# Kernel tuning notes

Hardware: AMD Instinct MI355X
Metric: run time of the kernel (lower is better)

The kernel has to match this reference:

```python
import jax, jax.numpy as jnp
import numpy as np

N_NODES = 100000
N_EDGES = 1600000
IN_FEATS = 64
HIDDEN = 64
NUM_CLASSES = 16


def setup_inputs() -> dict:
    key = jax.random.key(0)
    ks = jax.random.split(key, 8)
    features = jax.random.normal(ks[0], (N_NODES, IN_FEATS), dtype=jnp.float32)
    src = jax.random.randint(ks[1], (N_EDGES,), 0, N_NODES, dtype=jnp.int64)
    dst = jax.random.randint(ks[2], (N_EDGES,), 0, N_NODES, dtype=jnp.int64)
    W1 = jax.random.normal(ks[3], (IN_FEATS, HIDDEN), dtype=jnp.float32) * (1.0 / np.sqrt(IN_FEATS))
    b1 = jax.random.normal(ks[4], (HIDDEN,), dtype=jnp.float32) * 0.01
    W2 = jax.random.normal(ks[5], (HIDDEN, NUM_CLASSES), dtype=jnp.float32) * (1.0 / np.sqrt(HIDDEN))
    b2 = jax.random.normal(ks[6], (NUM_CLASSES,), dtype=jnp.float32) * 0.01
    return {"features": features, "src": src, "dst": dst,
            "W1": W1, "b1": b1, "W2": W2, "b2": b2}


def _mean_aggregate(x, src, dst, n_nodes):
    # gather source features along edges, segment-sum into destinations
    msg_sum = jax.ops.segment_sum(x[src], dst, num_segments=n_nodes)  # [N, d]
    deg = jax.ops.segment_sum(jnp.ones_like(dst, dtype=x.dtype), dst,
                              num_segments=n_nodes)                   # [N]
    # DGL mean leaves zero-in-degree nodes at 0; sum is already 0 there,
    # so clamping degree to 1 is exact.
    return msg_sum / jnp.maximum(deg, 1.0)[:, None]


def reference(features, src, dst, W1, b1, W2, b2):
    n = features.shape[0]
    h = _mean_aggregate(features, src, dst, n) @ W1 + b1   # GCNLayer 1
    h = jax.nn.relu(h)
    out = _mean_aggregate(h, src, dst, n) @ W2 + b2        # GCNLayer 2
    return out
```

## Files before the change

kernel.cpp:

```cpp
#include <hip/hip_runtime.h>
#include <hip/hip_fp16.h>

static constexpr int F = 64;
static constexpr int C = 16;
static constexpr int EPB = 2048;
static constexpr int BSH = 9;
static constexpr int SRCB = 17;
static constexpr int NPG = 4;

__global__ void prep(const float* __restrict__ x, __half* __restrict__ xh, int n4,
                     const int* __restrict__ dst, int* __restrict__ bucketCount,
                     int* __restrict__ blockHist, int nEdges) {
    int stride = gridDim.x * blockDim.x;
    for (int i = blockIdx.x * blockDim.x + threadIdx.x; i < n4; i += stride) {
        float4 v = ((const float4*)x)[i];
        __half2 p0 = __floats2half2_rn(v.x, v.y);
        __half2 p1 = __floats2half2_rn(v.z, v.w);
        uint2 o;
        o.x = *reinterpret_cast<unsigned*>(&p0);
        o.y = *reinterpret_cast<unsigned*>(&p1);
        ((uint2*)xh)[i] = o;
    }
    __shared__ int h[256];
    int t = threadIdx.x;
    h[t] = 0;
    __syncthreads();
    int e0 = blockIdx.x * EPB;
    for (int i = 0; i < EPB / 256; ++i) {
        int e = e0 + i * 256 + t;
        if (e < nEdges) atomicAdd(&h[dst[e] >> BSH], 1);
    }
    __syncthreads();
    blockHist[blockIdx.x * 256 + t] = h[t] ? atomicAdd(&bucketCount[t], h[t]) : 0;
}

__global__ void bucket_scan(const int* __restrict__ bucketCount,
                            int* __restrict__ bucketStart) {
    __shared__ int s[256];
    int t = threadIdx.x;
    s[t] = bucketCount[t];
    __syncthreads();
    for (int o = 1; o < 256; o <<= 1) {
        int v = (t >= o) ? s[t - o] : 0;
        __syncthreads();
        s[t] += v;
        __syncthreads();
    }
    bucketStart[t] = (t > 0) ? s[t - 1] : 0;
    if (t == 255) bucketStart[256] = s[255];
}

__global__ void partition(const int* __restrict__ src, const int* __restrict__ dst,
                          const int* __restrict__ blockHist,
                          const int* __restrict__ bucketStart,
                          unsigned* __restrict__ pairs, int nEdges) {
    __shared__ int base[256];
    __shared__ int rank[256];
    int t = threadIdx.x;
    rank[t] = 0;
    base[t] = bucketStart[t] + blockHist[blockIdx.x * 256 + t];
    __syncthreads();
    int e0 = blockIdx.x * EPB;
    for (int i = 0; i < EPB / 256; ++i) {
        int e = e0 + i * 256 + t;
        if (e < nEdges) {
            int d = dst[e];
            int b = d >> BSH;
            int r = atomicAdd(&rank[b], 1);
            pairs[base[b] + r] =
                ((unsigned)(d & ((1 << BSH) - 1)) << SRCB) | (unsigned)src[e];
        }
    }
}

__global__ void bucket_csr(const unsigned* __restrict__ pairs,
                           const int* __restrict__ bucketStart,
                           int* __restrict__ rowstart, int* __restrict__ csr,
                           int nNodes, int nEdges) {
    __shared__ int cnt[512];
    __shared__ int s[512];
    __shared__ int cur[512];
    int t = threadIdx.x;
    int b = blockIdx.x;
    int nodeBase = b << BSH;
    int pBeg = bucketStart[b], pEnd = bucketStart[b + 1];
    cnt[t] = 0;
    __syncthreads();
    for (int i = pBeg + t; i < pEnd; i += 512)
        atomicAdd(&cnt[pairs[i] >> SRCB], 1);
    __syncthreads();
    s[t] = cnt[t];
    __syncthreads();
    for (int o = 1; o < 512; o <<= 1) {
        int v = (t >= o) ? s[t - o] : 0;
        __syncthreads();
        s[t] += v;
        __syncthreads();
    }
    int rs = pBeg + ((t > 0) ? s[t - 1] : 0);
    int node = nodeBase + t;
    if (node < nNodes) rowstart[node] = rs;
    cur[t] = rs;
    __syncthreads();
    for (int i = pBeg + t; i < pEnd; i += 512) {
        unsigned p = pairs[i];
        int pos = atomicAdd(&cur[p >> SRCB], 1);
        csr[pos] = (int)(p & ((1u << SRCB) - 1));
    }
    if (b == 0 && t == 0) rowstart[nNodes] = nEdges;
}

__global__ void gather_h2(const __half* __restrict__ xh,
                          const int* __restrict__ rowstart,
                          const int* __restrict__ csr,
                          float* __restrict__ agg, int nNodes) {
    int gid = (blockIdx.x * blockDim.x + threadIdx.x) >> 4;
    int q = threadIdx.x & 15;
    int nodeBase = gid * NPG;
    if (nodeBase >= nNodes) return;
    const uint2* x2 = (const uint2*)xh;
    int rs[NPG + 1];
#pragma unroll
    for (int i = 0; i <= NPG; ++i) rs[i] = rowstart[min(nodeBase + i, nNodes)];
#pragma unroll
    for (int i = 0; i < NPG; ++i) {
        int node = nodeBase + i;
        if (node >= nNodes) break;
        int beg = rs[i], end = rs[i + 1];
        float4 a0 = make_float4(0.f, 0.f, 0.f, 0.f);
        float4 a1 = make_float4(0.f, 0.f, 0.f, 0.f);
        float4 a2 = make_float4(0.f, 0.f, 0.f, 0.f);
        float4 a3 = make_float4(0.f, 0.f, 0.f, 0.f);
        int k = beg;
        for (; k + 4 <= end; k += 4) {
            int s0 = csr[k], s1 = csr[k + 1], s2 = csr[k + 2], s3 = csr[k + 3];
            uint2 u0 = x2[(size_t)s0 * 16 + q];
            uint2 u1 = x2[(size_t)s1 * 16 + q];
            uint2 u2 = x2[(size_t)s2 * 16 + q];
            uint2 u3 = x2[(size_t)s3 * 16 + q];
            __half2 h00 = *reinterpret_cast<__half2*>(&u0.x);
            __half2 h01 = *reinterpret_cast<__half2*>(&u0.y);
            a0.x += __low2float(h00); a0.y += __high2float(h00);
            a0.z += __low2float(h01); a0.w += __high2float(h01);
            __half2 h10 = *reinterpret_cast<__half2*>(&u1.x);
            __half2 h11 = *reinterpret_cast<__half2*>(&u1.y);
            a1.x += __low2float(h10); a1.y += __high2float(h10);
            a1.z += __low2float(h11); a1.w += __high2float(h11);
            __half2 h20 = *reinterpret_cast<__half2*>(&u2.x);
            __half2 h21 = *reinterpret_cast<__half2*>(&u2.y);
            a2.x += __low2float(h20); a2.y += __high2float(h20);
            a2.z += __low2float(h21); a2.w += __high2float(h21);
            __half2 h30 = *reinterpret_cast<__half2*>(&u3.x);
            __half2 h31 = *reinterpret_cast<__half2*>(&u3.y);
            a3.x += __low2float(h30); a3.y += __high2float(h30);
            a3.z += __low2float(h31); a3.w += __high2float(h31);
        }
        for (; k < end; ++k) {
            int s0 = csr[k];
            uint2 u0 = x2[(size_t)s0 * 16 + q];
            __half2 h00 = *reinterpret_cast<__half2*>(&u0.x);
            __half2 h01 = *reinterpret_cast<__half2*>(&u0.y);
            a0.x += __low2float(h00); a0.y += __high2float(h00);
            a0.z += __low2float(h01); a0.w += __high2float(h01);
        }
        float inv = 1.0f / fmaxf((float)(end - beg), 1.0f);
        float4 o;
        o.x = ((a0.x + a1.x) + (a2.x + a3.x)) * inv;
        o.y = ((a0.y + a1.y) + (a2.y + a3.y)) * inv;
        o.z = ((a0.z + a1.z) + (a2.z + a3.z)) * inv;
        o.w = ((a0.w + a1.w) + (a2.w + a3.w)) * inv;
        ((float4*)agg)[(size_t)node * 16 + q] = o;
    }
}

__global__ void dense12_reg(const float* __restrict__ agg,
                            const float* __restrict__ W1,
                            const float* __restrict__ b1,
                            const float* __restrict__ W2,
                            __half* __restrict__ t2, int nNodes) {
    __shared__ float xs[4][F];
    __shared__ float hs[4][F];
    __shared__ float red[4][4][17];
    int wave = threadIdx.x >> 6, lane = threadIdx.x & 63;
    int kk = lane >> 4, c = lane & 15;

    float w1[F];
#pragma unroll
    for (int k = 0; k < F; ++k) w1[k] = W1[k * F + lane];
    float b1l = b1[lane];
    float w2[16];
#pragma unroll
    for (int j = 0; j < 16; ++j) w2[j] = W2[(kk * 16 + j) * C + c];

    int step = gridDim.x * 4;
    int start = blockIdx.x * 4 + wave;
    int iters = (nNodes + step - 1) / step;
    for (int i = 0; i < iters; ++i) {
        int node = start + i * step;
        bool live = node < nNodes;
        xs[wave][lane] = live ? agg[(size_t)node * F + lane] : 0.0f;
        __syncthreads();
        float hacc = b1l;
#pragma unroll
        for (int k = 0; k < F; ++k) hacc = fmaf(xs[wave][k], w1[k], hacc);
        hs[wave][lane] = fmaxf(hacc, 0.0f);
        __syncthreads();
        float p = 0.0f;
#pragma unroll
        for (int j = 0; j < 16; ++j) p = fmaf(hs[wave][kk * 16 + j], w2[j], p);
        red[wave][kk][c] = p;
        __syncthreads();
        if (lane < C && live) {
            float o = red[wave][0][lane] + red[wave][1][lane]
                    + red[wave][2][lane] + red[wave][3][lane];
            t2[(size_t)node * C + lane] = __float2half_rn(o);
        }
        __syncthreads();
    }
}

__global__ void gather16c(const __half* __restrict__ t2,
                          const int* __restrict__ rowstart,
                          const int* __restrict__ csr,
                          const float* __restrict__ b2,
                          float* __restrict__ out, int nNodes) {
    int gid = (blockIdx.x * blockDim.x + threadIdx.x) >> 4;
    int c = threadIdx.x & 15;
    int nodeBase = gid * NPG;
    if (nodeBase >= nNodes) return;
    float b2c = b2[c];
    int rs[NPG + 1];
#pragma unroll
    for (int i = 0; i <= NPG; ++i) rs[i] = rowstart[min(nodeBase + i, nNodes)];
#pragma unroll
    for (int i = 0; i < NPG; ++i) {
        int node = nodeBase + i;
        if (node >= nNodes) break;
        int beg = rs[i], end = rs[i + 1];
        float a0 = 0.f, a1 = 0.f, a2 = 0.f, a3 = 0.f;
        int k = beg;
        for (; k + 4 <= end; k += 4) {
            int s0 = csr[k], s1 = csr[k + 1], s2 = csr[k + 2], s3 = csr[k + 3];
            a0 += __half2float(t2[(size_t)s0 * C + c]);
            a1 += __half2float(t2[(size_t)s1 * C + c]);
            a2 += __half2float(t2[(size_t)s2 * C + c]);
            a3 += __half2float(t2[(size_t)s3 * C + c]);
        }
        for (; k < end; ++k) a0 += __half2float(t2[(size_t)csr[k] * C + c]);
        float d = fmaxf((float)(end - beg), 1.0f);
        out[(size_t)node * C + c] = ((a0 + a1) + (a2 + a3)) / d + b2c;
    }
}

extern "C" void kernel_launch(void* const* d_in, const int* in_sizes, int n_in,
                              void* d_out, int out_size, void* d_ws, size_t ws_size,
                              hipStream_t stream) {
    const float* features = (const float*)d_in[0];
    const int*   src      = (const int*)d_in[1];
    const int*   dst      = (const int*)d_in[2];
    const float* W1       = (const float*)d_in[3];
    const float* b1       = (const float*)d_in[4];
    const float* W2       = (const float*)d_in[5];
    const float* b2       = (const float*)d_in[6];
    float*       out      = (float*)d_out;

    const int nNodes = in_sizes[0] / F;
    const int nEdges = in_sizes[1];
    const int NBUCK = (nNodes + 511) >> BSH;
    const int NBLK  = (nEdges + EPB - 1) / EPB;

    char* ws = (char*)d_ws;
    auto align = [](size_t x) { return (x + 255) / 256 * 256; };
    int* bucketCount  = (int*)ws;    ws += align(256 * 4);
    int* bucketStart  = (int*)ws;    ws += align(257 * 4);
    int* blockHist    = (int*)ws;    ws += align((size_t)NBLK * 256 * 4);
    int* rowstart     = (int*)ws;    ws += align((size_t)(nNodes + 1) * 4);
    int* csr          = (int*)ws;    ws += align((size_t)nEdges * 4);
    __half* xh        = (__half*)ws; ws += align((size_t)nNodes * F * 2);
    float* agg        = (float*)ws;  ws += align((size_t)nNodes * F * 4);
    __half* t2h       = (__half*)ws; ws += align((size_t)nNodes * C * 2);
    unsigned* pairs   = (unsigned*)agg;

    hipMemsetAsync(bucketCount, 0, 256 * sizeof(int), stream);

    prep<<<NBLK, 256, 0, stream>>>(features, xh, nNodes * F / 4,
                                   dst, bucketCount, blockHist, nEdges);
    bucket_scan<<<1, 256, 0, stream>>>(bucketCount, bucketStart);
    partition<<<NBLK, 256, 0, stream>>>(src, dst, blockHist, bucketStart, pairs, nEdges);
    bucket_csr<<<NBUCK, 512, 0, stream>>>(pairs, bucketStart, rowstart, csr,
                                          nNodes, nEdges);

    {
        int nGroups = (nNodes + NPG - 1) / NPG;
        int blocks = (nGroups * 16 + 255) / 256;
        gather_h2<<<blocks, 256, 0, stream>>>(xh, rowstart, csr, agg, nNodes);
    }
    dense12_reg<<<2048, 256, 0, stream>>>(agg, W1, b1, W2, t2h, nNodes);

    {
        int nGroups = (nNodes + NPG - 1) / NPG;
        int blocks = (nGroups * 16 + 255) / 256;
        gather16c<<<blocks, 256, 0, stream>>>(t2h, rowstart, csr, b2, out, nNodes);
    }
}
```

Before: 151.7 us.

## Fold bucket scan into consumers and widen per-lane gather loads

Removes the single-block bucket_scan launch by recomputing the 256-entry prefix scan redundantly inside every partition and bucket_csr block. Both gather kernels now use wider per-lane loads: 16-byte half8 for layer 1 with 8 lanes per node, and 8-byte half4 for layer 2 with 4 lanes per node and float4 stores. The aim is fewer launches and fewer, larger memory transactions per gathered row. In exchange each block does extra scan work and barriers, and fewer threads per node means less parallelism per edge list.

```diff
diff --git a/kernel.cpp b/kernel.cpp
--- a/kernel.cpp
+++ b/kernel.cpp
@@ -34,31 +34,25 @@
     blockHist[blockIdx.x * 256 + t] = h[t] ? atomicAdd(&bucketCount[t], h[t]) : 0;
 }
 
-__global__ void bucket_scan(const int* __restrict__ bucketCount,
-                            int* __restrict__ bucketStart) {
-    __shared__ int s[256];
-    int t = threadIdx.x;
-    s[t] = bucketCount[t];
-    __syncthreads();
-    for (int o = 1; o < 256; o <<= 1) {
-        int v = (t >= o) ? s[t - o] : 0;
-        __syncthreads();
-        s[t] += v;
-        __syncthreads();
-    }
-    bucketStart[t] = (t > 0) ? s[t - 1] : 0;
-    if (t == 255) bucketStart[256] = s[255];
-}
-
 __global__ void partition(const int* __restrict__ src, const int* __restrict__ dst,
                           const int* __restrict__ blockHist,
-                          const int* __restrict__ bucketStart,
+                          const int* __restrict__ bucketCount,
                           unsigned* __restrict__ pairs, int nEdges) {
+    __shared__ int s[256];
     __shared__ int base[256];
     __shared__ int rank[256];
     int t = threadIdx.x;
+    s[t] = bucketCount[t];
     rank[t] = 0;
-    base[t] = bucketStart[t] + blockHist[blockIdx.x * 256 + t];
+    __syncthreads();
+    for (int o = 1; o < 256; o <<= 1) {
+        int v = (t >= o) ? s[t - o] : 0;
+        __syncthreads();
+        s[t] += v;
+        __syncthreads();
+    }
+    int bstart = (t > 0) ? s[t - 1] : 0;
+    base[t] = bstart + blockHist[blockIdx.x * 256 + t];
     __syncthreads();
     int e0 = blockIdx.x * EPB;
     for (int i = 0; i < EPB / 256; ++i) {
@@ -74,16 +68,26 @@
 }
 
 __global__ void bucket_csr(const unsigned* __restrict__ pairs,
-                           const int* __restrict__ bucketStart,
+                           const int* __restrict__ bucketCount,
                            int* __restrict__ rowstart, int* __restrict__ csr,
                            int nNodes, int nEdges) {
+    __shared__ int bscan[256];
     __shared__ int cnt[512];
     __shared__ int s[512];
     __shared__ int cur[512];
     int t = threadIdx.x;
     int b = blockIdx.x;
+    if (t < 256) bscan[t] = bucketCount[t];
+    __syncthreads();
+    for (int o = 1; o < 256; o <<= 1) {
+        int v = (t < 256 && t >= o) ? bscan[t - o] : 0;
+        __syncthreads();
+        if (t < 256) bscan[t] += v;
+        __syncthreads();
+    }
+    int pBeg = (b > 0) ? bscan[b - 1] : 0;
+    int pEnd = bscan[b];
     int nodeBase = b << BSH;
-    int pBeg = bucketStart[b], pEnd = bucketStart[b + 1];
     cnt[t] = 0;
     __syncthreads();
     for (int i = pBeg + t; i < pEnd; i += 512)
@@ -110,15 +114,26 @@
     if (b == 0 && t == 0) rowstart[nNodes] = nEdges;
 }
 
-__global__ void gather_h2(const __half* __restrict__ xh,
+__device__ __forceinline__ void acc8(float* a, uint4 u) {
+    __half2 h0 = *reinterpret_cast<__half2*>(&u.x);
+    __half2 h1 = *reinterpret_cast<__half2*>(&u.y);
+    __half2 h2 = *reinterpret_cast<__half2*>(&u.z);
+    __half2 h3 = *reinterpret_cast<__half2*>(&u.w);
+    a[0] += __low2float(h0); a[1] += __high2float(h0);
+    a[2] += __low2float(h1); a[3] += __high2float(h1);
+    a[4] += __low2float(h2); a[5] += __high2float(h2);
+    a[6] += __low2float(h3); a[7] += __high2float(h3);
+}
+
+__global__ void gather_h8(const __half* __restrict__ xh,
                           const int* __restrict__ rowstart,
                           const int* __restrict__ csr,
                           float* __restrict__ agg, int nNodes) {
-    int gid = (blockIdx.x * blockDim.x + threadIdx.x) >> 4;
-    int q = threadIdx.x & 15;
+    int gid = (blockIdx.x * blockDim.x + threadIdx.x) >> 3;
+    int q = threadIdx.x & 7;
     int nodeBase = gid * NPG;
     if (nodeBase >= nNodes) return;
-    const uint2* x2 = (const uint2*)xh;
+    const uint4* x4 = (const uint4*)xh;
     int rs[NPG + 1];
 #pragma unroll
     for (int i = 0; i <= NPG; ++i) rs[i] = rowstart[min(nodeBase + i, nNodes)];
@@ -127,49 +142,33 @@
         int node = nodeBase + i;
         if (node >= nNodes) break;
         int beg = rs[i], end = rs[i + 1];
-        float4 a0 = make_float4(0.f, 0.f, 0.f, 0.f);
-        float4 a1 = make_float4(0.f, 0.f, 0.f, 0.f);
-        float4 a2 = make_float4(0.f, 0.f, 0.f, 0.f);
-        float4 a3 = make_float4(0.f, 0.f, 0.f, 0.f);
+        float a0[8] = {0,0,0,0,0,0,0,0};
+        float a1[8] = {0,0,0,0,0,0,0,0};
+        float a2[8] = {0,0,0,0,0,0,0,0};
+        float a3[8] = {0,0,0,0,0,0,0,0};
         int k = beg;
         for (; k + 4 <= end; k += 4) {
             int s0 = csr[k], s1 = csr[k + 1], s2 = csr[k + 2], s3 = csr[k + 3];
-            uint2 u0 = x2[(size_t)s0 * 16 + q];
-            uint2 u1 = x2[(size_t)s1 * 16 + q];
-            uint2 u2 = x2[(size_t)s2 * 16 + q];
-            uint2 u3 = x2[(size_t)s3 * 16 + q];
-            __half2 h00 = *reinterpret_cast<__half2*>(&u0.x);
-            __half2 h01 = *reinterpret_cast<__half2*>(&u0.y);
-            a0.x += __low2float(h00); a0.y += __high2float(h00);
-            a0.z += __low2float(h01); a0.w += __high2float(h01);
-            __half2 h10 = *reinterpret_cast<__half2*>(&u1.x);
-            __half2 h11 = *reinterpret_cast<__half2*>(&u1.y);
-            a1.x += __low2float(h10); a1.y += __high2float(h10);
-            a1.z += __low2float(h11); a1.w += __high2float(h11);
-            __half2 h20 = *reinterpret_cast<__half2*>(&u2.x);
-            __half2 h21 = *reinterpret_cast<__half2*>(&u2.y);
-            a2.x += __low2float(h20); a2.y += __high2float(h20);
-            a2.z += __low2float(h21); a2.w += __high2float(h21);
-            __half2 h30 = *reinterpret_cast<__half2*>(&u3.x);
-            __half2 h31 = *reinterpret_cast<__half2*>(&u3.y);
-            a3.x += __low2float(h30); a3.y += __high2float(h30);
-            a3.z += __low2float(h31); a3.w += __high2float(h31);
-        }
-        for (; k < end; ++k) {
-            int s0 = csr[k];
-            uint2 u0 = x2[(size_t)s0 * 16 + q];
-            __half2 h00 = *reinterpret_cast<__half2*>(&u0.x);
-            __half2 h01 = *reinterpret_cast<__half2*>(&u0.y);
-            a0.x += __low2float(h00); a0.y += __high2float(h00);
-            a0.z += __low2float(h01); a0.w += __high2float(h01);
-        }
+            uint4 u0 = x4[(size_t)s0 * 8 + q];
+            uint4 u1 = x4[(size_t)s1 * 8 + q];
+            uint4 u2 = x4[(size_t)s2 * 8 + q];
+            uint4 u3 = x4[(size_t)s3 * 8 + q];
+            acc8(a0, u0); acc8(a1, u1); acc8(a2, u2); acc8(a3, u3);
+        }
+        for (; k < end; ++k)
+            acc8(a0, x4[(size_t)csr[k] * 8 + q]);
         float inv = 1.0f / fmaxf((float)(end - beg), 1.0f);
-        float4 o;
-        o.x = ((a0.x + a1.x) + (a2.x + a3.x)) * inv;
-        o.y = ((a0.y + a1.y) + (a2.y + a3.y)) * inv;
-        o.z = ((a0.z + a1.z) + (a2.z + a3.z)) * inv;
-        o.w = ((a0.w + a1.w) + (a2.w + a3.w)) * inv;
-        ((float4*)agg)[(size_t)node * 16 + q] = o;
+        float4 o0, o1;
+        o0.x = ((a0[0] + a1[0]) + (a2[0] + a3[0])) * inv;
+        o0.y = ((a0[1] + a1[1]) + (a2[1] + a3[1])) * inv;
+        o0.z = ((a0[2] + a1[2]) + (a2[2] + a3[2])) * inv;
+        o0.w = ((a0[3] + a1[3]) + (a2[3] + a3[3])) * inv;
+        o1.x = ((a0[4] + a1[4]) + (a2[4] + a3[4])) * inv;
+        o1.y = ((a0[5] + a1[5]) + (a2[5] + a3[5])) * inv;
+        o1.z = ((a0[6] + a1[6]) + (a2[6] + a3[6])) * inv;
+        o1.w = ((a0[7] + a1[7]) + (a2[7] + a3[7])) * inv;
+        ((float4*)agg)[(size_t)node * 16 + q * 2]     = o0;
+        ((float4*)agg)[(size_t)node * 16 + q * 2 + 1] = o1;
     }
 }
 
@@ -219,16 +218,17 @@
     }
 }
 
-__global__ void gather16c(const __half* __restrict__ t2,
-                          const int* __restrict__ rowstart,
-                          const int* __restrict__ csr,
-                          const float* __restrict__ b2,
-                          float* __restrict__ out, int nNodes) {
-    int gid = (blockIdx.x * blockDim.x + threadIdx.x) >> 4;
-    int c = threadIdx.x & 15;
+__global__ void gather16_4(const __half* __restrict__ t2,
+                           const int* __restrict__ rowstart,
+                           const int* __restrict__ csr,
+                           const float* __restrict__ b2,
+                           float* __restrict__ out, int nNodes) {
+    int gid = (blockIdx.x * blockDim.x + threadIdx.x) >> 2;
+    int q = threadIdx.x & 3;
     int nodeBase = gid * NPG;
     if (nodeBase >= nNodes) return;
-    float b2c = b2[c];
+    const uint2* t2v = (const uint2*)t2;
+    float4 b2v = ((const float4*)b2)[q];
     int rs[NPG + 1];
 #pragma unroll
     for (int i = 0; i <= NPG; ++i) rs[i] = rowstart[min(nodeBase + i, nNodes)];
@@ -237,18 +237,43 @@
         int node = nodeBase + i;
         if (node >= nNodes) break;
         int beg = rs[i], end = rs[i + 1];
-        float a0 = 0.f, a1 = 0.f, a2 = 0.f, a3 = 0.f;
+        float a0[4] = {0,0,0,0}, a1[4] = {0,0,0,0};
+        float a2[4] = {0,0,0,0}, a3[4] = {0,0,0,0};
         int k = beg;
         for (; k + 4 <= end; k += 4) {
             int s0 = csr[k], s1 = csr[k + 1], s2 = csr[k + 2], s3 = csr[k + 3];
-            a0 += __half2float(t2[(size_t)s0 * C + c]);
-            a1 += __half2float(t2[(size_t)s1 * C + c]);
-            a2 += __half2float(t2[(size_t)s2 * C + c]);
-            a3 += __half2float(t2[(size_t)s3 * C + c]);
-        }
-        for (; k < end; ++k) a0 += __half2float(t2[(size_t)csr[k] * C + c]);
-        float d = fmaxf((float)(end - beg), 1.0f);
-        out[(size_t)node * C + c] = ((a0 + a1) + (a2 + a3)) / d + b2c;
+            uint2 u0 = t2v[(size_t)s0 * 4 + q];
+            uint2 u1 = t2v[(size_t)s1 * 4 + q];
+            uint2 u2 = t2v[(size_t)s2 * 4 + q];
+            uint2 u3 = t2v[(size_t)s3 * 4 + q];
+            __half2 p, r;
+            p = *reinterpret_cast<__half2*>(&u0.x); r = *reinterpret_cast<__half2*>(&u0.y);
+            a0[0] += __low2float(p); a0[1] += __high2float(p);
+            a0[2] += __low2float(r); a0[3] += __high2float(r);
+            p = *reinterpret_cast<__half2*>(&u1.x); r = *reinterpret_cast<__half2*>(&u1.y);
+            a1[0] += __low2float(p); a1[1] += __high2float(p);
+            a1[2] += __low2float(r); a1[3] += __high2float(r);
+            p = *reinterpret_cast<__half2*>(&u2.x); r = *reinterpret_cast<__half2*>(&u2.y);
+            a2[0] += __low2float(p); a2[1] += __high2float(p);
+            a2[2] += __low2float(r); a2[3] += __high2float(r);
+            p = *reinterpret_cast<__half2*>(&u3.x); r = *reinterpret_cast<__half2*>(&u3.y);
+            a3[0] += __low2float(p); a3[1] += __high2float(p);
+            a3[2] += __low2float(r); a3[3] += __high2float(r);
+        }
+        for (; k < end; ++k) {
+            uint2 u0 = t2v[(size_t)csr[k] * 4 + q];
+            __half2 p = *reinterpret_cast<__half2*>(&u0.x);
+            __half2 r = *reinterpret_cast<__half2*>(&u0.y);
+            a0[0] += __low2float(p); a0[1] += __high2float(p);
+            a0[2] += __low2float(r); a0[3] += __high2float(r);
+        }
+        float dinv = 1.0f / fmaxf((float)(end - beg), 1.0f);
+        float4 o;
+        o.x = ((a0[0] + a1[0]) + (a2[0] + a3[0])) * dinv + b2v.x;
+        o.y = ((a0[1] + a1[1]) + (a2[1] + a3[1])) * dinv + b2v.y;
+        o.z = ((a0[2] + a1[2]) + (a2[2] + a3[2])) * dinv + b2v.z;
+        o.w = ((a0[3] + a1[3]) + (a2[3] + a3[3])) * dinv + b2v.w;
+        ((float4*)out)[(size_t)node * 4 + q] = o;
     }
 }
 
@@ -272,7 +297,6 @@
     char* ws = (char*)d_ws;
     auto align = [](size_t x) { return (x + 255) / 256 * 256; };
     int* bucketCount  = (int*)ws;    ws += align(256 * 4);
-    int* bucketStart  = (int*)ws;    ws += align(257 * 4);
     int* blockHist    = (int*)ws;    ws += align((size_t)NBLK * 256 * 4);
     int* rowstart     = (int*)ws;    ws += align((size_t)(nNodes + 1) * 4);
     int* csr          = (int*)ws;    ws += align((size_t)nEdges * 4);
@@ -285,21 +309,20 @@
 
     prep<<<NBLK, 256, 0, stream>>>(features, xh, nNodes * F / 4,
                                    dst, bucketCount, blockHist, nEdges);
-    bucket_scan<<<1, 256, 0, stream>>>(bucketCount, bucketStart);
-    partition<<<NBLK, 256, 0, stream>>>(src, dst, blockHist, bucketStart, pairs, nEdges);
-    bucket_csr<<<NBUCK, 512, 0, stream>>>(pairs, bucketStart, rowstart, csr,
+    partition<<<NBLK, 256, 0, stream>>>(src, dst, blockHist, bucketCount, pairs, nEdges);
+    bucket_csr<<<NBUCK, 512, 0, stream>>>(pairs, bucketCount, rowstart, csr,
                                           nNodes, nEdges);
 
     {
         int nGroups = (nNodes + NPG - 1) / NPG;
-        int blocks = (nGroups * 16 + 255) / 256;
-        gather_h2<<<blocks, 256, 0, stream>>>(xh, rowstart, csr, agg, nNodes);
+        int blocks = (nGroups * 8 + 255) / 256;
+        gather_h8<<<blocks, 256, 0, stream>>>(xh, rowstart, csr, agg, nNodes);
     }
     dense12_reg<<<2048, 256, 0, stream>>>(agg, W1, b1, W2, t2h, nNodes);
 
     {
         int nGroups = (nNodes + NPG - 1) / NPG;
-        int blocks = (nGroups * 16 + 255) / 256;
-        gather16c<<<blocks, 256, 0, stream>>>(t2h, rowstart, csr, b2, out, nNodes);
-    }
-}
+        int blocks = (nGroups * 4 + 255) / 256;
+        gather16_4<<<blocks, 256, 0, stream>>>(t2h, rowstart, csr, b2, out, nNodes);
+    }
+}
```

Result: slower. 157.3 us (+3.7%).
